# Performance work log

Hardware: AMD Instinct MI355X
Metric: run time of the kernel (lower is better)

Reference implementation:

```python
import jax, jax.numpy as jnp
import numpy as np

IMG = 224      # image height/width
P = 4          # patch size
R = 16         # number of superpixels (SLIC num_segments)
B = 32         # batch
D = 768        # embed dim


def setup_inputs() -> dict:
    key = jax.random.key(0)
    k1, k2 = jax.random.split(key)
    n_patches = (IMG // P) ** 2  # 3136
    patch_embeddings = jax.random.normal(k1, (B, n_patches, D), dtype=jnp.float32)
    segmentation_map = jax.random.randint(k2, (B, IMG, IMG), 0, R, dtype=jnp.int32)
    return {
        "patch_embeddings": patch_embeddings,
        "segmentation_map": segmentation_map,
        "patch_size": P,
        "num_segments": R,
    }


def _dominant_segment_ids(segmentation_map, patch_size, num_segments):
    # Vectorized PatchToSuperpixelMapper.map_patches: per-patch mode of labels.
    Bm, H, W = segmentation_map.shape
    npx = H // patch_size
    # [B, npx, p, npx, p] -> [B, N, p*p] pixels per patch
    pix = (segmentation_map
           .reshape(Bm, npx, patch_size, npx, patch_size)
           .transpose(0, 1, 3, 2, 4)
           .reshape(Bm, npx * npx, patch_size * patch_size))
    # histogram over segment labels; argmax tie-breaks to smallest label,
    # matching torch.unique (sorted) + counts.argmax.
    counts = jnp.sum(pix[..., None] == jnp.arange(num_segments, dtype=pix.dtype), axis=2)  # [B, N, R]
    return jnp.argmax(counts, axis=-1)  # [B, N] int


def reference(patch_embeddings, segmentation_map, patch_size, num_segments):
    # SuperpixelPooling('mean').pool driven by map_patches, fully vectorized.
    Bm, N, Dm = patch_embeddings.shape
    seg_ids = _dominant_segment_ids(segmentation_map, patch_size, num_segments)  # [B, N]
    # offset segment ids per batch element -> single segment_sum over B*R bins
    flat_ids = (seg_ids + jnp.arange(Bm, dtype=seg_ids.dtype)[:, None] * num_segments).reshape(-1)
    sums = jax.ops.segment_sum(patch_embeddings.reshape(Bm * N, Dm), flat_ids,
                               num_segments=Bm * num_segments)            # [B*R, D]
    cnt = jax.ops.segment_sum(jnp.ones((Bm * N,), patch_embeddings.dtype), flat_ids,
                              num_segments=Bm * num_segments)             # [B*R]
    pooled = sums / jnp.maximum(cnt, 1.0)[:, None]  # empty superpixels stay zero
    return pooled.reshape(Bm, num_segments, Dm)
```

## Files before the change

kernel.cpp:

```cpp
#include <hip/hip_runtime.h>

#define IMG 224
#define PSZ 4
#define NPX (IMG / PSZ)
#define NPATCH (NPX * NPX)
#define BB 32
#define RR 16
#define DD 768
#define NCHUNK 32
#define CHUNK (NPATCH / NCHUNK)
#define T2 192

template <bool ATOMIC>
__global__ __launch_bounds__(T2) void k_pool(const float* __restrict__ emb,
                                             const int* __restrict__ segmap,
                                             int* __restrict__ counts,
                                             float* __restrict__ dst) {
    const int blk = blockIdx.x;
    const int b = blk / NCHUNK;
    const int c = blk - b * NCHUNK;
    const int n0 = c * CHUNK;

    __shared__ int sseg[CHUNK];
    __shared__ int lcnt[RR];
    if (threadIdx.x < RR) lcnt[threadIdx.x] = 0;
    __syncthreads();

    for (int i = threadIdx.x; i < CHUNK; i += T2) {
        int n = n0 + i;
        int py = n / NPX, px = n - py * NPX;
        const int* base = segmap + ((size_t)b * IMG + (size_t)py * PSZ) * IMG + px * PSZ;
        unsigned long long lo = 0ull, hi = 0ull;
#pragma unroll
        for (int j = 0; j < PSZ; j++) {
            int4 v = *(const int4*)(base + (size_t)j * IMG);
            int ss[4] = {v.x, v.y, v.z, v.w};
#pragma unroll
            for (int k = 0; k < 4; k++) {
                int s = ss[k];
                unsigned long long inc = 1ull << ((s & 7) * 8);
                if (s < 8) lo += inc; else hi += inc;
            }
        }
        int best = 0, bc = -1;
#pragma unroll
        for (int r = 0; r < RR; r++) {
            unsigned long long word = (r < 8) ? lo : hi;
            int cc = (int)((word >> ((r & 7) * 8)) & 0xffull);
            if (cc > bc) { bc = cc; best = r; }
        }
        sseg[i] = best;
        atomicAdd(&lcnt[best], 1);
    }
    __syncthreads();
    if (threadIdx.x < RR)
        atomicAdd(&counts[b * RR + threadIdx.x], lcnt[threadIdx.x]);

    const int t = threadIdx.x;
    const float* src = emb + ((size_t)(b * NPATCH + n0)) * DD + t * 4;

    float4 acc[RR];
#pragma unroll
    for (int r = 0; r < RR; r++) acc[r] = make_float4(0.f, 0.f, 0.f, 0.f);

#pragma unroll 1
    for (int p = 0; p < CHUNK - 2; p += 4) {
        float4 v0 = *(const float4*)(src + (size_t)(p + 0) * DD);
        float4 v1 = *(const float4*)(src + (size_t)(p + 1) * DD);
        float4 v2 = *(const float4*)(src + (size_t)(p + 2) * DD);
        float4 v3 = *(const float4*)(src + (size_t)(p + 3) * DD);
        int s0 = sseg[p + 0], s1 = sseg[p + 1], s2 = sseg[p + 2], s3 = sseg[p + 3];
#pragma unroll
        for (int r = 0; r < RR; r++) {
            float w0 = (s0 == r) ? 1.f : 0.f;
            float w1 = (s1 == r) ? 1.f : 0.f;
            float w2 = (s2 == r) ? 1.f : 0.f;
            float w3 = (s3 == r) ? 1.f : 0.f;
            acc[r].x = fmaf(w0, v0.x, acc[r].x);
            acc[r].y = fmaf(w0, v0.y, acc[r].y);
            acc[r].z = fmaf(w0, v0.z, acc[r].z);
            acc[r].w = fmaf(w0, v0.w, acc[r].w);
            acc[r].x = fmaf(w1, v1.x, acc[r].x);
            acc[r].y = fmaf(w1, v1.y, acc[r].y);
            acc[r].z = fmaf(w1, v1.z, acc[r].z);
            acc[r].w = fmaf(w1, v1.w, acc[r].w);
            acc[r].x = fmaf(w2, v2.x, acc[r].x);
            acc[r].y = fmaf(w2, v2.y, acc[r].y);
            acc[r].z = fmaf(w2, v2.z, acc[r].z);
            acc[r].w = fmaf(w2, v2.w, acc[r].w);
            acc[r].x = fmaf(w3, v3.x, acc[r].x);
            acc[r].y = fmaf(w3, v3.y, acc[r].y);
            acc[r].z = fmaf(w3, v3.z, acc[r].z);
            acc[r].w = fmaf(w3, v3.w, acc[r].w);
        }
    }
    {
        const int p = CHUNK - 2;
        float4 v0 = *(const float4*)(src + (size_t)(p + 0) * DD);
        float4 v1 = *(const float4*)(src + (size_t)(p + 1) * DD);
        int s0 = sseg[p + 0], s1 = sseg[p + 1];
#pragma unroll
        for (int r = 0; r < RR; r++) {
            float w0 = (s0 == r) ? 1.f : 0.f;
            float w1 = (s1 == r) ? 1.f : 0.f;
            acc[r].x = fmaf(w0, v0.x, acc[r].x);
            acc[r].y = fmaf(w0, v0.y, acc[r].y);
            acc[r].z = fmaf(w0, v0.z, acc[r].z);
            acc[r].w = fmaf(w0, v0.w, acc[r].w);
            acc[r].x = fmaf(w1, v1.x, acc[r].x);
            acc[r].y = fmaf(w1, v1.y, acc[r].y);
            acc[r].z = fmaf(w1, v1.z, acc[r].z);
            acc[r].w = fmaf(w1, v1.w, acc[r].w);
        }
    }

    if (ATOMIC) {
        float* o = dst + ((size_t)b * RR) * DD + t * 4;
#pragma unroll
        for (int r = 0; r < RR; r++) {
            atomicAdd(o + r * DD + 0, acc[r].x);
            atomicAdd(o + r * DD + 1, acc[r].y);
            atomicAdd(o + r * DD + 2, acc[r].z);
            atomicAdd(o + r * DD + 3, acc[r].w);
        }
    } else {
        float* o = dst + (((size_t)c * BB + b) * RR) * DD + t * 4;
#pragma unroll
        for (int r = 0; r < RR; r++)
            *(float4*)(o + r * DD) = acc[r];
    }
}

__global__ __launch_bounds__(T2) void k_finish_part(const float* __restrict__ part,
                                                    const int* __restrict__ counts,
                                                    float* __restrict__ out) {
    const int br = blockIdx.x;
    const int t = threadIdx.x;
    const float* p0 = part + (size_t)br * DD + t * 4;
    float4 s = make_float4(0.f, 0.f, 0.f, 0.f);
#pragma unroll
    for (int c = 0; c < NCHUNK; c++) {
        float4 v = *(const float4*)(p0 + (size_t)c * (BB * RR * DD));
        s.x += v.x; s.y += v.y; s.z += v.z; s.w += v.w;
    }
    float inv = 1.f / fmaxf((float)counts[br], 1.f);
    float4 o = make_float4(s.x * inv, s.y * inv, s.z * inv, s.w * inv);
    *(float4*)(out + (size_t)br * DD + t * 4) = o;
}

__global__ __launch_bounds__(256) void k_finish_atomic(const int* __restrict__ counts,
                                                       float* __restrict__ out) {
    int e = blockIdx.x * 256 + threadIdx.x;
    if (e >= BB * RR * DD) return;
    float cnt = (float)counts[e / DD];
    out[e] = out[e] / fmaxf(cnt, 1.f);
}

extern "C" void kernel_launch(void* const* d_in, const int* in_sizes, int n_in,
                              void* d_out, int out_size, void* d_ws, size_t ws_size,
                              hipStream_t stream) {
    const float* emb = (const float*)d_in[0];
    const int* segmap = (const int*)d_in[1];
    (void)in_sizes; (void)n_in; (void)out_size;

    char* ws = (char*)d_ws;
    int* counts = (int*)ws;
    float* part = (float*)(ws + 2048);
    const size_t need = 2048 + (size_t)NCHUNK * BB * RR * DD * sizeof(float);
    float* out = (float*)d_out;

    hipMemsetAsync(counts, 0, BB * RR * sizeof(int), stream);

    if (ws_size >= need) {
        k_pool<false><<<BB * NCHUNK, T2, 0, stream>>>(emb, segmap, counts, part);
        k_finish_part<<<BB * RR, T2, 0, stream>>>(part, counts, out);
    } else {
        hipMemsetAsync(out, 0, (size_t)BB * RR * DD * sizeof(float), stream);
        k_pool<true><<<BB * NCHUNK, T2, 0, stream>>>(emb, segmap, counts, out);
        k_finish_atomic<<<(BB * RR * DD + 255) / 256, 256, 0, stream>>>(counts, out);
    }
}
```

Before: 437.9 us.

## Split embed dim across two blocks and halve patch chunks per batch

Each pooling block now covers half the embedding dimension with float2 loads, and each covers a chunk twice as long. The grid size stays the same. Fewer chunks halve the partial-sum workspace written by the pool kernel and read by the finish kernel. Halving the accumulator array lowers register pressure. The cost is that both D-halves recompute the per-patch dominant segment from the segmentation map, and each lane issues narrower loads.

```diff
diff --git a/kernel.cpp b/kernel.cpp
--- a/kernel.cpp
+++ b/kernel.cpp
@@ -7,8 +7,10 @@
 #define BB 32
 #define RR 16
 #define DD 768
-#define NCHUNK 32
+#define NCHUNK 16
 #define CHUNK (NPATCH / NCHUNK)
+#define DSPLIT 2
+#define DHALF (DD / DSPLIT)
 #define T2 192
 
 template <bool ATOMIC>
@@ -17,8 +19,10 @@
                                              int* __restrict__ counts,
                                              float* __restrict__ dst) {
     const int blk = blockIdx.x;
-    const int b = blk / NCHUNK;
-    const int c = blk - b * NCHUNK;
+    const int dh = blk & (DSPLIT - 1);
+    const int bc = blk >> 1;
+    const int b = bc / NCHUNK;
+    const int c = bc - b * NCHUNK;
     const int n0 = c * CHUNK;
 
     __shared__ int sseg[CHUNK];
@@ -42,33 +46,33 @@
                 if (s < 8) lo += inc; else hi += inc;
             }
         }
-        int best = 0, bc = -1;
+        int best = 0, bcount = -1;
 #pragma unroll
         for (int r = 0; r < RR; r++) {
             unsigned long long word = (r < 8) ? lo : hi;
             int cc = (int)((word >> ((r & 7) * 8)) & 0xffull);
-            if (cc > bc) { bc = cc; best = r; }
+            if (cc > bcount) { bcount = cc; best = r; }
         }
         sseg[i] = best;
-        atomicAdd(&lcnt[best], 1);
+        if (dh == 0) atomicAdd(&lcnt[best], 1);
     }
     __syncthreads();
-    if (threadIdx.x < RR)
+    if (dh == 0 && threadIdx.x < RR)
         atomicAdd(&counts[b * RR + threadIdx.x], lcnt[threadIdx.x]);
 
     const int t = threadIdx.x;
-    const float* src = emb + ((size_t)(b * NPATCH + n0)) * DD + t * 4;
+    const float* src = emb + ((size_t)(b * NPATCH + n0)) * DD + dh * DHALF + t * 2;
 
-    float4 acc[RR];
+    float2 acc[RR];
 #pragma unroll
-    for (int r = 0; r < RR; r++) acc[r] = make_float4(0.f, 0.f, 0.f, 0.f);
+    for (int r = 0; r < RR; r++) acc[r] = make_float2(0.f, 0.f);
 
 #pragma unroll 1
-    for (int p = 0; p < CHUNK - 2; p += 4) {
-        float4 v0 = *(const float4*)(src + (size_t)(p + 0) * DD);
-        float4 v1 = *(const float4*)(src + (size_t)(p + 1) * DD);
-        float4 v2 = *(const float4*)(src + (size_t)(p + 2) * DD);
-        float4 v3 = *(const float4*)(src + (size_t)(p + 3) * DD);
+    for (int p = 0; p < CHUNK; p += 4) {
+        float2 v0 = *(const float2*)(src + (size_t)(p + 0) * DD);
+        float2 v1 = *(const float2*)(src + (size_t)(p + 1) * DD);
+        float2 v2 = *(const float2*)(src + (size_t)(p + 2) * DD);
+        float2 v3 = *(const float2*)(src + (size_t)(p + 3) * DD);
         int s0 = sseg[p + 0], s1 = sseg[p + 1], s2 = sseg[p + 2], s3 = sseg[p + 3];
 #pragma unroll
         for (int r = 0; r < RR; r++) {
@@ -78,56 +82,27 @@
             float w3 = (s3 == r) ? 1.f : 0.f;
             acc[r].x = fmaf(w0, v0.x, acc[r].x);
             acc[r].y = fmaf(w0, v0.y, acc[r].y);
-            acc[r].z = fmaf(w0, v0.z, acc[r].z);
-            acc[r].w = fmaf(w0, v0.w, acc[r].w);
             acc[r].x = fmaf(w1, v1.x, acc[r].x);
             acc[r].y = fmaf(w1, v1.y, acc[r].y);
-            acc[r].z = fmaf(w1, v1.z, acc[r].z);
-            acc[r].w = fmaf(w1, v1.w, acc[r].w);
             acc[r].x = fmaf(w2, v2.x, acc[r].x);
             acc[r].y = fmaf(w2, v2.y, acc[r].y);
-            acc[r].z = fmaf(w2, v2.z, acc[r].z);
-            acc[r].w = fmaf(w2, v2.w, acc[r].w);
             acc[r].x = fmaf(w3, v3.x, acc[r].x);
             acc[r].y = fmaf(w3, v3.y, acc[r].y);
-            acc[r].z = fmaf(w3, v3.z, acc[r].z);
-            acc[r].w = fmaf(w3, v3.w, acc[r].w);
-        }
-    }
-    {
-        const int p = CHUNK - 2;
-        float4 v0 = *(const float4*)(src + (size_t)(p + 0) * DD);
-        float4 v1 = *(const float4*)(src + (size_t)(p + 1) * DD);
-        int s0 = sseg[p + 0], s1 = sseg[p + 1];
-#pragma unroll
-        for (int r = 0; r < RR; r++) {
-            float w0 = (s0 == r) ? 1.f : 0.f;
-            float w1 = (s1 == r) ? 1.f : 0.f;
-            acc[r].x = fmaf(w0, v0.x, acc[r].x);
-            acc[r].y = fmaf(w0, v0.y, acc[r].y);
-            acc[r].z = fmaf(w0, v0.z, acc[r].z);
-            acc[r].w = fmaf(w0, v0.w, acc[r].w);
-            acc[r].x = fmaf(w1, v1.x, acc[r].x);
-            acc[r].y = fmaf(w1, v1.y, acc[r].y);
-            acc[r].z = fmaf(w1, v1.z, acc[r].z);
-            acc[r].w = fmaf(w1, v1.w, acc[r].w);
         }
     }
 
     if (ATOMIC) {
-        float* o = dst + ((size_t)b * RR) * DD + t * 4;
+        float* o = dst + ((size_t)b * RR) * DD + dh * DHALF + t * 2;
 #pragma unroll
         for (int r = 0; r < RR; r++) {
             atomicAdd(o + r * DD + 0, acc[r].x);
             atomicAdd(o + r * DD + 1, acc[r].y);
-            atomicAdd(o + r * DD + 2, acc[r].z);
-            atomicAdd(o + r * DD + 3, acc[r].w);
         }
     } else {
-        float* o = dst + (((size_t)c * BB + b) * RR) * DD + t * 4;
+        float* o = dst + (((size_t)c * BB + b) * RR) * DD + dh * DHALF + t * 2;
 #pragma unroll
         for (int r = 0; r < RR; r++)
-            *(float4*)(o + r * DD) = acc[r];
+            *(float2*)(o + r * DD) = acc[r];
     }
 }
 
@@ -172,11 +147,11 @@
     hipMemsetAsync(counts, 0, BB * RR * sizeof(int), stream);
 
     if (ws_size >= need) {
-        k_pool<false><<<BB * NCHUNK, T2, 0, stream>>>(emb, segmap, counts, part);
+        k_pool<false><<<BB * NCHUNK * DSPLIT, T2, 0, stream>>>(emb, segmap, counts, part);
         k_finish_part<<<BB * RR, T2, 0, stream>>>(part, counts, out);
     } else {
         hipMemsetAsync(out, 0, (size_t)BB * RR * DD * sizeof(float), stream);
-        k_pool<true><<<BB * NCHUNK, T2, 0, stream>>>(emb, segmap, counts, out);
+        k_pool<true><<<BB * NCHUNK * DSPLIT, T2, 0, stream>>>(emb, segmap, counts, out);
         k_finish_atomic<<<(BB * RR * DD + 255) / 256, 256, 0, stream>>>(counts, out);
     }
 }
```

After: 440.3 us. No clear change (+0.6%).
